# Performance work log

Measured on AMD Instinct MI355X. Metric: run time of the kernel, lower is better.

The kernel has to match this reference:

```python
import jax, jax.numpy as jnp
import numpy as np

HS_ENC, HS_DEC, ATTN = 1024, 1024, 1024
N, T = 32, 2048


def setup_inputs() -> dict:
    key = jax.random.key(0)
    k1, k2, k3, k4, k5, k6 = jax.random.split(key, 6)
    h_dec = jax.random.normal(k1, (N, HS_DEC), dtype=jnp.float32)
    h_enc = jax.random.normal(k2, (N, T, HS_ENC), dtype=jnp.float32)
    src_lens = jax.random.randint(k3, (N,), 1, T + 1, dtype=jnp.int32)
    # params of nn.Linear(hs_enc+hs_dec, attn_size) and score vector v
    W = jax.random.normal(k4, (ATTN, HS_DEC + HS_ENC), dtype=jnp.float32) * 0.02
    b = jax.random.normal(k5, (ATTN,), dtype=jnp.float32) * 0.02
    v = jax.random.normal(k6, (ATTN,), dtype=jnp.float32)
    return {"h_dec": h_dec, "h_enc": h_enc, "src_lens": src_lens, "W": W, "b": b, "v": v}


def reference(h_dec, h_enc, src_lens, W, b, v):
    # Linear over concat(h_dec, h_enc) == sum of split projections; avoids
    # materializing the repeated/concatenated [N, T, hs_dec+hs_enc] tensor.
    hs_dec = h_dec.shape[-1]
    Wd, We = W[:, :hs_dec], W[:, hs_dec:]          # [A, hs_dec], [A, hs_enc]
    dec_proj = jnp.einsum('nd,ad->na', h_dec, Wd)  # [N, A]
    enc_proj = jnp.einsum('nte,ae->nta', h_enc, We)  # [N, T, A]
    attn_out = jnp.tanh(dec_proj[:, None, :] + enc_proj + b)  # [N, T, A]
    score = jnp.einsum('nta,a->nt', attn_out, v)   # [N, T]
    T_ = h_enc.shape[1]
    mask = jnp.arange(T_)[None, :] < src_lens[:, None]
    score = jnp.where(mask, score, jnp.float32(-1e10))
    weights = jax.nn.softmax(score, axis=-1)       # [N, T]
    ctx = jnp.einsum('nt,nte->ne', weights, h_enc) # [N, hs_enc]
    return ctx, weights
```

## Files before the change

### kernel.cpp

```cpp
#include <hip/hip_runtime.h>
#include <hip/hip_fp16.h>

#define HS 1024
#define TT 2048

typedef _Float16 half8 __attribute__((ext_vector_type(8)));
typedef float floatx4 __attribute__((ext_vector_type(4)));

__device__ __forceinline__ void dma16(const _Float16* g, _Float16* l) {
    __builtin_amdgcn_global_load_lds(
        (const __attribute__((address_space(1))) unsigned int*)g,
        (__attribute__((address_space(3))) unsigned int*)l, 16, 0, 0);
}

__global__ __launch_bounds__(256) void k_dproj(const float* __restrict__ h_dec,
                                               const float* __restrict__ W,
                                               const float* __restrict__ bias,
                                               float* __restrict__ dproj) {
    int wid = blockIdx.x * 4 + (threadIdx.x >> 6);
    int lane = threadIdx.x & 63;
    int n = wid >> 10, a = wid & 1023;
    const float4* hd = reinterpret_cast<const float4*>(h_dec + (size_t)n * HS);
    const float4* wr = reinterpret_cast<const float4*>(W + (size_t)a * 2048);
    float s = 0.f;
#pragma unroll
    for (int i = 0; i < 4; ++i) {
        float4 h = hd[lane + i * 64];
        float4 w = wr[lane + i * 64];
        s += h.x * w.x + h.y * w.y + h.z * w.z + h.w * w.w;
    }
    for (int off = 32; off; off >>= 1) s += __shfl_xor(s, off);
    if (lane == 0) dproj[wid] = bias[a] + s;
}

__global__ __launch_bounds__(256) void k_cvtW(const float* __restrict__ W,
                                              _Float16* __restrict__ We16) {
    int idx4 = (blockIdx.x * 256 + threadIdx.x) * 4;
    int a = idx4 >> 10;
    int e = idx4 & 1023;
    float4 f = *reinterpret_cast<const float4*>(W + (size_t)a * 2048 + 1024 + e);
    _Float16 h0 = (_Float16)f.x, h1 = (_Float16)f.y, h2 = (_Float16)f.z, h3 = (_Float16)f.w;
    ushort4 p;
    p.x = *(unsigned short*)&h0; p.y = *(unsigned short*)&h1;
    p.z = *(unsigned short*)&h2; p.w = *(unsigned short*)&h3;
    *reinterpret_cast<ushort4*>(We16 + idx4) = p;
}

__global__ __launch_bounds__(256) void k_cvtA(const float* __restrict__ h_enc,
                                              _Float16* __restrict__ h_enc16) {
    size_t idx = ((size_t)blockIdx.x * 256 + threadIdx.x) * 16;
    const float4* g = reinterpret_cast<const float4*>(h_enc + idx);
    _Float16 h[16];
#pragma unroll
    for (int i = 0; i < 4; ++i) {
        float4 f = g[i];
        h[i * 4 + 0] = (_Float16)f.x; h[i * 4 + 1] = (_Float16)f.y;
        h[i * 4 + 2] = (_Float16)f.z; h[i * 4 + 3] = (_Float16)f.w;
    }
    *reinterpret_cast<uint4*>(h_enc16 + idx)     = *reinterpret_cast<uint4*>(&h[0]);
    *reinterpret_cast<uint4*>(h_enc16 + idx + 8) = *reinterpret_cast<uint4*>(&h[8]);
}

__global__ __launch_bounds__(256, 2) void k_score(const _Float16* __restrict__ h_enc16,
                                                  const _Float16* __restrict__ We16,
                                                  const float* __restrict__ dproj,
                                                  const float* __restrict__ v,
                                                  float* __restrict__ scores) {
    __shared__ _Float16 Asb[2][128 * 32];
    __shared__ _Float16 Bsb[2][256 * 32];
    __shared__ float s_acc[128];

    const int tid = threadIdx.x;
    const int n  = blockIdx.x >> 4;
    const int t0 = (blockIdx.x & 15) << 7;

    if (tid < 128) s_acc[tid] = 0.0f;

    const int w    = tid >> 6;
    const int lane = tid & 63;
    const int wm = w >> 1, wn = w & 1;
    const int col = lane & 15, quad = lane >> 4;

    const int lrow = lane >> 2;
    const int lg   = (lane & 3) ^ ((lrow >> 1) & 3);
    const size_t goff = (size_t)lrow * HS + lg * 8;

    const _Float16* gA = h_enc16 + (size_t)(n * TT + t0) * HS + goff;
    const _Float16* gB = We16 + goff;

    floatx4 acc[4][8];
    float vv[8], dd[8];

    auto issue = [&](int it, int p) {
        const int a0 = (it >> 5) << 8;
        const int kk = (it & 31) << 5;
        const _Float16* gAi = gA + kk;
        const _Float16* gBi = gB + (size_t)a0 * HS + kk;
#pragma unroll
        for (int j = 0; j < 2; ++j)
            dma16(gAi + (size_t)(w * 32 + j * 16) * HS, &Asb[p][(w * 2 + j) * 512]);
#pragma unroll
        for (int j = 0; j < 4; ++j)
            dma16(gBi + (size_t)(w * 64 + j * 16) * HS, &Bsb[p][(w * 4 + j) * 512]);
    };

    issue(0, 0);

    for (int it = 0; it < 128; ++it) {
        const int p = it & 1;

        __syncthreads();

        if (it + 1 < 128) issue(it + 1, 1 - p);

        if ((it & 31) == 0) {
            const int a0 = (it >> 5) << 8;
#pragma unroll
            for (int ni = 0; ni < 8; ++ni) {
                int a = a0 + wn * 128 + ni * 16 + col;
                vv[ni] = v[a];
                dd[ni] = dproj[n * HS + a];
            }
#pragma unroll
            for (int mi = 0; mi < 4; ++mi)
#pragma unroll
                for (int ni = 0; ni < 8; ++ni)
                    acc[mi][ni] = (floatx4)0.0f;
        }

        const _Float16* Ab = Asb[p];
        const _Float16* Bb = Bsb[p];
        half8 af[4], bf[8];
#pragma unroll
        for (int mi = 0; mi < 4; ++mi) {
            const int r = wm * 64 + mi * 16 + col;
            af[mi] = *reinterpret_cast<const half8*>(
                &Ab[r * 32 + ((quad ^ ((r >> 1) & 3)) << 3)]);
        }
#pragma unroll
        for (int ni = 0; ni < 8; ++ni) {
            const int r = wn * 128 + ni * 16 + col;
            bf[ni] = *reinterpret_cast<const half8*>(
                &Bb[r * 32 + ((quad ^ ((r >> 1) & 3)) << 3)]);
        }
#pragma unroll
        for (int mi = 0; mi < 4; ++mi)
#pragma unroll
            for (int ni = 0; ni < 8; ++ni)
                acc[mi][ni] = __builtin_amdgcn_mfma_f32_16x16x32_f16(
                    af[mi], bf[ni], acc[mi][ni], 0, 0, 0);

        if ((it & 31) == 31) {
#pragma unroll
            for (int mi = 0; mi < 4; ++mi) {
#pragma unroll
                for (int rg = 0; rg < 4; ++rg) {
                    float s = 0.0f;
#pragma unroll
                    for (int ni = 0; ni < 8; ++ni) {
                        float x = acc[mi][ni][rg] + dd[ni];
                        float e2 = __expf(2.0f * x);
                        float th = 1.0f - 2.0f * __builtin_amdgcn_rcpf(e2 + 1.0f);
                        s += vv[ni] * th;
                    }
                    s += __shfl_xor(s, 8);
                    s += __shfl_xor(s, 4);
                    s += __shfl_xor(s, 2);
                    s += __shfl_xor(s, 1);
                    if (col == 0)
                        atomicAdd(&s_acc[wm * 64 + mi * 16 + quad * 4 + rg], s);
                }
            }
        }
    }
    __syncthreads();
    if (tid < 128) scores[(size_t)n * TT + t0 + tid] = s_acc[tid];
}

__global__ __launch_bounds__(256) void k_softmax(float* __restrict__ wout,
                                                 const int* __restrict__ lens) {
    __shared__ float red[4];
    __shared__ float red2[4];
    int n = blockIdx.x, tid = threadIdx.x;
    int len = lens[n];
    float* row = wout + (size_t)n * TT;
    float sv[8];
    float m = -3.0e38f;
#pragma unroll
    for (int i = 0; i < 8; ++i) {
        int t = tid + i * 256;
        float s = row[t];
        s = (t < len) ? s : -1.0e10f;
        sv[i] = s;
        m = fmaxf(m, s);
    }
    for (int off = 1; off <= 32; off <<= 1) m = fmaxf(m, __shfl_xor(m, off));
    if ((tid & 63) == 0) red[tid >> 6] = m;
    __syncthreads();
    m = fmaxf(fmaxf(red[0], red[1]), fmaxf(red[2], red[3]));
    float sum = 0.f, es[8];
#pragma unroll
    for (int i = 0; i < 8; ++i) { es[i] = __expf(sv[i] - m); sum += es[i]; }
    for (int off = 1; off <= 32; off <<= 1) sum += __shfl_xor(sum, off);
    if ((tid & 63) == 0) red2[tid >> 6] = sum;
    __syncthreads();
    sum = red2[0] + red2[1] + red2[2] + red2[3];
    float rinv = 1.0f / sum;
#pragma unroll
    for (int i = 0; i < 8; ++i) row[tid + i * 256] = es[i] * rinv;
}

__global__ __launch_bounds__(256) void k_ctx(const _Float16* __restrict__ h_enc16,
                                             const float* __restrict__ wts,
                                             float* __restrict__ ctx) {
    __shared__ float red[256][8];
    int b = blockIdx.x;
    int n  = b >> 4;
    int ec = (b >> 2) & 3;
    int ts = b & 3;
    int tid = threadIdx.x;
    int q = tid & 31, tg = tid >> 5;
    int e = ec * 256 + q * 8;
    float acc[8];
#pragma unroll
    for (int j = 0; j < 8; ++j) acc[j] = 0.f;
    const float* wrow = wts + (size_t)n * TT;
    for (int t = ts * 512 + tg; t < ts * 512 + 512; t += 8) {
        float w = wrow[t];
        uint4 raw = *reinterpret_cast<const uint4*>(
            h_enc16 + ((size_t)(n * TT + t)) * HS + e);
        const _Float16* hp = reinterpret_cast<const _Float16*>(&raw);
#pragma unroll
        for (int j = 0; j < 8; ++j) acc[j] += w * (float)hp[j];
    }
#pragma unroll
    for (int j = 0; j < 8; ++j) red[tid][j] = acc[j];
    __syncthreads();
    if (tid < 32) {
        float s[8];
#pragma unroll
        for (int j = 0; j < 8; ++j) s[j] = red[tid][j];
        for (int g = 1; g < 8; ++g)
#pragma unroll
            for (int j = 0; j < 8; ++j) s[j] += red[g * 32 + tid][j];
        float* dst = ctx + (size_t)n * HS + ec * 256 + tid * 8;
#pragma unroll
        for (int j = 0; j < 8; ++j) atomicAdd(dst + j, s[j]);
    }
}

__global__ __launch_bounds__(256) void k_score_naive(const float* __restrict__ h_enc,
                                                     const float* __restrict__ W,
                                                     const float* __restrict__ dproj,
                                                     const float* __restrict__ v,
                                                     float* __restrict__ scores) {
    int gw = blockIdx.x * 4 + (threadIdx.x >> 6);
    int lane = threadIdx.x & 63;
    int n = gw >> 11, t = gw & 2047;
    const float4* he = reinterpret_cast<const float4*>(h_enc + ((size_t)(n * TT + t)) * HS);
    float4 hv[4];
#pragma unroll
    for (int i = 0; i < 4; ++i) hv[i] = he[lane + i * 64];
    float s = 0.f;
    for (int a = 0; a < 1024; ++a) {
        const float4* wr = reinterpret_cast<const float4*>(W + (size_t)a * 2048 + 1024);
        float d = 0.f;
#pragma unroll
        for (int i = 0; i < 4; ++i) {
            float4 wv = wr[lane + i * 64];
            d += hv[i].x * wv.x + hv[i].y * wv.y + hv[i].z * wv.z + hv[i].w * wv.w;
        }
        for (int off = 32; off; off >>= 1) d += __shfl_xor(d, off);
        s += v[a] * tanhf(d + dproj[n * HS + a]);
    }
    if (lane == 0) scores[(size_t)n * TT + t] = s;
}

__global__ __launch_bounds__(256) void k_ctx_naive(const float* __restrict__ h_enc,
                                                   const float* __restrict__ wts,
                                                   float* __restrict__ ctx) {
    int n = blockIdx.x;
    int e = threadIdx.x * 4;
    float4 a = make_float4(0.f, 0.f, 0.f, 0.f);
    const float* wrow = wts + (size_t)n * TT;
    for (int t = 0; t < TT; ++t) {
        float w = wrow[t];
        float4 h = *reinterpret_cast<const float4*>(h_enc + ((size_t)(n * TT + t)) * HS + e);
        a.x += w * h.x; a.y += w * h.y; a.z += w * h.z; a.w += w * h.w;
    }
    *reinterpret_cast<float4*>(ctx + (size_t)n * HS + e) = a;
}

extern "C" void kernel_launch(void* const* d_in, const int* in_sizes, int n_in,
                              void* d_out, int out_size, void* d_ws, size_t ws_size,
                              hipStream_t stream) {
    const float* h_dec    = (const float*)d_in[0];
    const float* h_enc    = (const float*)d_in[1];
    const int*   src_lens = (const int*)d_in[2];
    const float* W = (const float*)d_in[3];
    const float* b = (const float*)d_in[4];
    const float* v = (const float*)d_in[5];

    float* out = (float*)d_out;
    float* ctx = out;
    float* wts = out + 32 * 1024;

    float*    dproj   = (float*)d_ws;
    _Float16* We16    = (_Float16*)((char*)d_ws + 131072);
    _Float16* h_enc16 = (_Float16*)((char*)d_ws + 131072 + 2097152);
    const size_t need = 131072 + 2097152 + (size_t)32 * TT * HS * 2;

    k_dproj<<<8192, 256, 0, stream>>>(h_dec, W, b, dproj);
    if (ws_size >= need) {
        (void)hipMemsetAsync(ctx, 0, 32 * 1024 * sizeof(float), stream);
        k_cvtW <<<1024, 256, 0, stream>>>(W, We16);
        k_cvtA <<<16384, 256, 0, stream>>>(h_enc, h_enc16);
        k_score<<<512, 256, 0, stream>>>(h_enc16, We16, dproj, v, wts);
        k_softmax<<<32, 256, 0, stream>>>(wts, src_lens);
        k_ctx  <<<512, 256, 0, stream>>>(h_enc16, wts, ctx);
    } else {
        k_score_naive<<<16384, 256, 0, stream>>>(h_enc, W, dproj, v, wts);
        k_softmax<<<32, 256, 0, stream>>>(wts, src_lens);
        k_ctx_naive<<<32, 256, 0, stream>>>(h_enc, wts, ctx);
    }
}
```

Measured before the change: 594.6 us.

## Rewrite score GEMM as 256x256 tiles with 8 waves and 4-stage pipeline

Replaces the score kernel with a 512-thread block computing a 256(T)x256(A) tile over full K, using a 4-deep global_load_lds ring buffer with explicit vmcnt waits, interleaved DMA issue between MFMA halves, and s_setprio around MFMA bursts. The attention dimension is split across blocks, so partial scores are combined with global atomicAdd into a pre-zeroed weights buffer (an extra memset). Block IDs are remapped for L2 locality. The aim is higher MFMA utilization and better latency hiding, at the cost of larger LDS (128KB per block) and nondeterministic summation order.

```diff
diff --git a/kernel.cpp b/kernel.cpp
--- a/kernel.cpp
+++ b/kernel.cpp
@@ -61,120 +61,134 @@
     *reinterpret_cast<uint4*>(h_enc16 + idx + 8) = *reinterpret_cast<uint4*>(&h[8]);
 }
 
-__global__ __launch_bounds__(256, 2) void k_score(const _Float16* __restrict__ h_enc16,
-                                                  const _Float16* __restrict__ We16,
-                                                  const float* __restrict__ dproj,
-                                                  const float* __restrict__ v,
-                                                  float* __restrict__ scores) {
-    __shared__ _Float16 Asb[2][128 * 32];
-    __shared__ _Float16 Bsb[2][256 * 32];
-    __shared__ float s_acc[128];
+__global__ __launch_bounds__(512, 2) void k_score8(
+        const _Float16* __restrict__ h_enc16, const _Float16* __restrict__ We16,
+        const float* __restrict__ dproj, const float* __restrict__ v,
+        float* __restrict__ scores) {
+    __shared__ _Float16 As[4][256 * 32];
+    __shared__ _Float16 Bs[4][256 * 32];
+    __shared__ float s_acc[256];
 
     const int tid = threadIdx.x;
-    const int n  = blockIdx.x >> 4;
-    const int t0 = (blockIdx.x & 15) << 7;
-
-    if (tid < 128) s_acc[tid] = 0.0f;
-
-    const int w    = tid >> 6;
-    const int lane = tid & 63;
-    const int wm = w >> 1, wn = w & 1;
+    const int ord = ((blockIdx.x & 7) << 7) | (blockIdx.x >> 3);
+    const int aT = ord & 3, tT = (ord >> 2) & 7, n = ord >> 5;
+    const int t0 = tT << 8, a0 = aT << 8;
+
+    if (tid < 256) s_acc[tid] = 0.0f;
+
+    const int w = tid >> 6, lane = tid & 63;
+    const int wm = w >> 2, wn = w & 3;
     const int col = lane & 15, quad = lane >> 4;
 
-    const int lrow = lane >> 2;
-    const int lg   = (lane & 3) ^ ((lrow >> 1) & 3);
-    const size_t goff = (size_t)lrow * HS + lg * 8;
-
-    const _Float16* gA = h_enc16 + (size_t)(n * TT + t0) * HS + goff;
-    const _Float16* gB = We16 + goff;
-
-    floatx4 acc[4][8];
-    float vv[8], dd[8];
-
-    auto issue = [&](int it, int p) {
-        const int a0 = (it >> 5) << 8;
-        const int kk = (it & 31) << 5;
-        const _Float16* gAi = gA + kk;
-        const _Float16* gBi = gB + (size_t)a0 * HS + kk;
-#pragma unroll
-        for (int j = 0; j < 2; ++j)
-            dma16(gAi + (size_t)(w * 32 + j * 16) * HS, &Asb[p][(w * 2 + j) * 512]);
-#pragma unroll
-        for (int j = 0; j < 4; ++j)
-            dma16(gBi + (size_t)(w * 64 + j * 16) * HS, &Bsb[p][(w * 4 + j) * 512]);
+    const _Float16* srcA[2];
+    const _Float16* srcB[2];
+#pragma unroll
+    for (int c = 0; c < 2; ++c) {
+        int Gp = c * 512 + tid;
+        int Gl = Gp ^ ((Gp >> 3) & 7);
+        int r = Gl >> 2, g = Gl & 3;
+        srcA[c] = h_enc16 + ((size_t)(n * TT + t0 + r)) * HS + g * 8;
+        srcB[c] = We16 + ((size_t)(a0 + r)) * HS + g * 8;
+    }
+
+    int offA[8], offB[4];
+#pragma unroll
+    for (int mi = 0; mi < 8; ++mi) {
+        int r = wm * 128 + mi * 16 + col;
+        offA[mi] = (r * 64 + quad * 16) ^ (((r >> 1) & 7) << 4);
+    }
+#pragma unroll
+    for (int ni = 0; ni < 4; ++ni) {
+        int r = wn * 64 + ni * 16 + col;
+        offB[ni] = (r * 64 + quad * 16) ^ (((r >> 1) & 7) << 4);
+    }
+
+    floatx4 acc[8][4];
+#pragma unroll
+    for (int mi = 0; mi < 8; ++mi)
+#pragma unroll
+        for (int ni = 0; ni < 4; ++ni) acc[mi][ni] = (floatx4)0.0f;
+
+    auto issue2 = [&](int kt, int c) {
+        const int b = kt & 3;
+        dma16(srcA[c] + kt * 32, &As[b][c * 4096 + w * 512]);
+        dma16(srcB[c] + kt * 32, &Bs[b][c * 4096 + w * 512]);
     };
 
-    issue(0, 0);
-
-    for (int it = 0; it < 128; ++it) {
-        const int p = it & 1;
-
-        __syncthreads();
-
-        if (it + 1 < 128) issue(it + 1, 1 - p);
-
-        if ((it & 31) == 0) {
-            const int a0 = (it >> 5) << 8;
-#pragma unroll
-            for (int ni = 0; ni < 8; ++ni) {
-                int a = a0 + wn * 128 + ni * 16 + col;
-                vv[ni] = v[a];
-                dd[ni] = dproj[n * HS + a];
-            }
-#pragma unroll
-            for (int mi = 0; mi < 4; ++mi)
-#pragma unroll
-                for (int ni = 0; ni < 8; ++ni)
-                    acc[mi][ni] = (floatx4)0.0f;
-        }
-
-        const _Float16* Ab = Asb[p];
-        const _Float16* Bb = Bsb[p];
-        half8 af[4], bf[8];
-#pragma unroll
-        for (int mi = 0; mi < 4; ++mi) {
-            const int r = wm * 64 + mi * 16 + col;
-            af[mi] = *reinterpret_cast<const half8*>(
-                &Ab[r * 32 + ((quad ^ ((r >> 1) & 3)) << 3)]);
-        }
-#pragma unroll
-        for (int ni = 0; ni < 8; ++ni) {
-            const int r = wn * 128 + ni * 16 + col;
-            bf[ni] = *reinterpret_cast<const half8*>(
-                &Bb[r * 32 + ((quad ^ ((r >> 1) & 3)) << 3)]);
-        }
+#pragma unroll
+    for (int kt = 0; kt < 3; ++kt) { issue2(kt, 0); issue2(kt, 1); }
+
+    for (int kt = 0; kt < 32; ++kt) {
+        const int b = kt & 3;
+        if (kt < 30)       asm volatile("s_waitcnt vmcnt(8)" ::: "memory");
+        else if (kt == 30) asm volatile("s_waitcnt vmcnt(4)" ::: "memory");
+        else               asm volatile("s_waitcnt vmcnt(0)" ::: "memory");
+        __builtin_amdgcn_s_barrier();
+        __builtin_amdgcn_sched_barrier(0);
+
+        const char* Ab = (const char*)As[b];
+        const char* Bb = (const char*)Bs[b];
+        half8 af[4], bf[4];
+#pragma unroll
+        for (int ni = 0; ni < 4; ++ni)
+            bf[ni] = *reinterpret_cast<const half8*>(Bb + offB[ni]);
 #pragma unroll
         for (int mi = 0; mi < 4; ++mi)
-#pragma unroll
-            for (int ni = 0; ni < 8; ++ni)
+            af[mi] = *reinterpret_cast<const half8*>(Ab + offA[mi]);
+        if (kt < 29) issue2(kt + 3, 0);
+        __builtin_amdgcn_s_setprio(1);
+#pragma unroll
+        for (int mi = 0; mi < 4; ++mi)
+#pragma unroll
+            for (int ni = 0; ni < 4; ++ni)
                 acc[mi][ni] = __builtin_amdgcn_mfma_f32_16x16x32_f16(
                     af[mi], bf[ni], acc[mi][ni], 0, 0, 0);
-
-        if ((it & 31) == 31) {
-#pragma unroll
-            for (int mi = 0; mi < 4; ++mi) {
-#pragma unroll
-                for (int rg = 0; rg < 4; ++rg) {
-                    float s = 0.0f;
-#pragma unroll
-                    for (int ni = 0; ni < 8; ++ni) {
-                        float x = acc[mi][ni][rg] + dd[ni];
-                        float e2 = __expf(2.0f * x);
-                        float th = 1.0f - 2.0f * __builtin_amdgcn_rcpf(e2 + 1.0f);
-                        s += vv[ni] * th;
-                    }
-                    s += __shfl_xor(s, 8);
-                    s += __shfl_xor(s, 4);
-                    s += __shfl_xor(s, 2);
-                    s += __shfl_xor(s, 1);
-                    if (col == 0)
-                        atomicAdd(&s_acc[wm * 64 + mi * 16 + quad * 4 + rg], s);
-                }
+        __builtin_amdgcn_s_setprio(0);
+
+#pragma unroll
+        for (int mi = 0; mi < 4; ++mi)
+            af[mi] = *reinterpret_cast<const half8*>(Ab + offA[4 + mi]);
+        if (kt < 29) issue2(kt + 3, 1);
+        __builtin_amdgcn_s_setprio(1);
+#pragma unroll
+        for (int mi = 0; mi < 4; ++mi)
+#pragma unroll
+            for (int ni = 0; ni < 4; ++ni)
+                acc[4 + mi][ni] = __builtin_amdgcn_mfma_f32_16x16x32_f16(
+                    af[mi], bf[ni], acc[4 + mi][ni], 0, 0, 0);
+        __builtin_amdgcn_s_setprio(0);
+    }
+
+    float vv[4], dd[4];
+#pragma unroll
+    for (int ni = 0; ni < 4; ++ni) {
+        const int a = a0 + wn * 64 + ni * 16 + col;
+        vv[ni] = v[a];
+        dd[ni] = dproj[n * HS + a];
+    }
+#pragma unroll
+    for (int mi = 0; mi < 8; ++mi) {
+#pragma unroll
+        for (int rg = 0; rg < 4; ++rg) {
+            float s = 0.0f;
+#pragma unroll
+            for (int ni = 0; ni < 4; ++ni) {
+                float x = acc[mi][ni][rg] + dd[ni];
+                float e2 = __expf(2.0f * x);
+                float th = 1.0f - 2.0f * __builtin_amdgcn_rcpf(e2 + 1.0f);
+                s += vv[ni] * th;
             }
+            s += __shfl_xor(s, 8);
+            s += __shfl_xor(s, 4);
+            s += __shfl_xor(s, 2);
+            s += __shfl_xor(s, 1);
+            if (col == 0)
+                atomicAdd(&s_acc[wm * 128 + mi * 16 + quad * 4 + rg], s);
         }
     }
     __syncthreads();
-    if (tid < 128) scores[(size_t)n * TT + t0 + tid] = s_acc[tid];
+    if (tid < 256)
+        atomicAdd(&scores[(size_t)n * TT + t0 + tid], s_acc[tid]);
 }
 
 __global__ __launch_bounds__(256) void k_softmax(float* __restrict__ wout,
@@ -313,9 +327,10 @@
     k_dproj<<<8192, 256, 0, stream>>>(h_dec, W, b, dproj);
     if (ws_size >= need) {
         (void)hipMemsetAsync(ctx, 0, 32 * 1024 * sizeof(float), stream);
+        (void)hipMemsetAsync(wts, 0, (size_t)32 * TT * sizeof(float), stream);
         k_cvtW <<<1024, 256, 0, stream>>>(W, We16);
         k_cvtA <<<16384, 256, 0, stream>>>(h_enc, h_enc16);
-        k_score<<<512, 256, 0, stream>>>(h_enc16, We16, dproj, v, wts);
+        k_score8<<<1024, 512, 0, stream>>>(h_enc16, We16, dproj, v, wts);
         k_softmax<<<32, 256, 0, stream>>>(wts, src_lens);
         k_ctx  <<<512, 256, 0, stream>>>(h_enc16, wts, ctx);
     } else {
```

Result: no change. 599.7 us (+0.9%).
